# Kernel optimization log

Hardware: AMD Instinct MI355X
Metric: run time of the kernel (lower is better)

Reference implementation:

```python
import jax, jax.numpy as jnp
import numpy as np

B, T, IN, H, OUT = 128, 512, 64, 512, 1
H2 = H // 2


def setup_inputs() -> dict:
    key = jax.random.key(0)
    ks = jax.random.split(key, 16)
    s_in = 1.0 / np.sqrt(H)  # torch LSTM/Linear init scale ~ U(-1/sqrt(H), 1/sqrt(H))
    def u(k, shape, s):
        return jax.random.uniform(k, shape, jnp.float32, -s, s)
    return {
        "x": jax.random.normal(ks[0], (B, T, IN), jnp.float32),
        "W_ih0": u(ks[1], (4 * H, IN), s_in),
        "W_hh0": u(ks[2], (4 * H, H), s_in),
        "b_ih0": u(ks[3], (4 * H,), s_in),
        "b_hh0": u(ks[4], (4 * H,), s_in),
        "W_ih1": u(ks[5], (4 * H, H), s_in),
        "W_hh1": u(ks[6], (4 * H, H), s_in),
        "b_ih1": u(ks[7], (4 * H,), s_in),
        "b_hh1": u(ks[8], (4 * H,), s_in),
        "fc1_w": u(ks[9], (H2, H), s_in),
        "fc1_b": u(ks[10], (H2,), s_in),
        "fc2_w": u(ks[11], (OUT, H2), 1.0 / np.sqrt(H2)),
        "fc2_b": u(ks[12], (OUT,), 1.0 / np.sqrt(H2)),
    }


def _lstm_layer(x, W_ih, W_hh, b_ih, b_hh):
    # x: [B, T, D_in] -> outputs h for all timesteps [B, T, H]
    b, t, _ = x.shape
    h_dim = W_hh.shape[1]
    # precompute input contribution to gates for all timesteps: [T, B, 4H]
    xg = (jnp.einsum('btd,gd->btg', x, W_ih) + b_ih + b_hh).transpose(1, 0, 2)

    def step(carry, xt):
        h, c = carry
        gates = xt + h @ W_hh.T  # [B, 4H]
        i, f, g, o = jnp.split(gates, 4, axis=-1)  # torch gate order i,f,g,o
        i = jax.nn.sigmoid(i)
        f = jax.nn.sigmoid(f)
        g = jnp.tanh(g)
        o = jax.nn.sigmoid(o)
        c = f * c + i * g
        h = o * jnp.tanh(c)
        return (h, c), h

    h0 = jnp.zeros((b, h_dim), x.dtype)
    (_, _), hs = jax.lax.scan(step, (h0, h0), xg)
    return hs.transpose(1, 0, 2)  # [B, T, H]


def reference(x, W_ih0, W_hh0, b_ih0, b_hh0, W_ih1, W_hh1, b_ih1, b_hh1,
              fc1_w, fc1_b, fc2_w, fc2_b):
    h1 = _lstm_layer(x, W_ih0, W_hh0, b_ih0, b_hh0)
    h2 = _lstm_layer(h1, W_ih1, W_hh1, b_ih1, b_hh1)
    last = h2[:, -1, :]  # [B, H]
    z = jax.nn.relu(last @ fc1_w.T + fc1_b)
    return z @ fc2_w.T + fc2_b  # [B, OUT]
```

## Files before the change

kernel.cpp:

```cpp
#include <hip/hip_runtime.h>
#include <hip/hip_fp16.h>

#define BB   128
#define TT   512
#define INS  64
#define HH   512
#define K0   576
#define K1   1024
#define PAD0 584
#define PAD1 1032
#define NWG  128
#define NTHR 512
#define H2   256

typedef _Float16 f16;
typedef f16 f16x4 __attribute__((ext_vector_type(4)));
typedef f16 f16x8 __attribute__((ext_vector_type(8)));
typedef float f32x4 __attribute__((ext_vector_type(4)));

__device__ __forceinline__ float sigmoidf_(float x) {
  return 1.0f / (1.0f + __expf(-x));
}
__device__ __forceinline__ float tanhf_(float x) {
  return 1.0f - 2.0f / (__expf(2.0f * x) + 1.0f);
}

__device__ __forceinline__ f16x8 ldg_h(const f16* p) {
  union { unsigned long long q[2]; f16x8 v; } u;
  const unsigned long long* qp = (const unsigned long long*)p;
  u.q[0] = __hip_atomic_load(qp,     __ATOMIC_RELAXED, __HIP_MEMORY_SCOPE_AGENT);
  u.q[1] = __hip_atomic_load(qp + 1, __ATOMIC_RELAXED, __HIP_MEMORY_SCOPE_AGENT);
  return u.v;
}
__device__ __forceinline__ void stg_h(f16* p, unsigned int pk) {
  __hip_atomic_store((unsigned int*)p, pk, __ATOMIC_RELAXED, __HIP_MEMORY_SCOPE_AGENT);
}

__global__ __launch_bounds__(NTHR, 1) void lstm_fused(
    const float* __restrict__ x,
    const float* __restrict__ Wih0, const float* __restrict__ Whh0,
    const float* __restrict__ bih0, const float* __restrict__ bhh0,
    const float* __restrict__ Wih1, const float* __restrict__ Whh1,
    const float* __restrict__ bih1, const float* __restrict__ bhh1,
    int* __restrict__ bar, f16* __restrict__ h1buf, f16* __restrict__ h2buf)
{
  extern __shared__ f16 smem[];
  f16* W0s = smem;
  f16* W1s = smem + 32 * PAD0;

  const int tid  = threadIdx.x;
  const int wg   = blockIdx.x;
  const int mg   = wg >> 6;
  const int ng   = wg & 63;
  const int wid  = tid >> 6;
  const int lane = tid & 63;

  for (int e4 = tid; e4 < 32 * (K0 / 4); e4 += NTHR) {
    int r = e4 / (K0 / 4), k = (e4 - r * (K0 / 4)) * 4;
    int g = ((r >> 3) << 9) + (ng << 3) + (r & 7);
    float4 v = (k < INS)
        ? *reinterpret_cast<const float4*>(Wih0 + g * INS + k)
        : *reinterpret_cast<const float4*>(Whh0 + g * HH + (k - INS));
    f16x4 h; h[0]=(f16)v.x; h[1]=(f16)v.y; h[2]=(f16)v.z; h[3]=(f16)v.w;
    *reinterpret_cast<f16x4*>(&W0s[r * PAD0 + k]) = h;
  }
  for (int e4 = tid; e4 < 32 * (K1 / 4); e4 += NTHR) {
    int r = e4 >> 8, k = (e4 & 255) * 4;
    int g = ((r >> 3) << 9) + (ng << 3) + (r & 7);
    float4 v = (k < HH)
        ? *reinterpret_cast<const float4*>(Wih1 + g * HH + k)
        : *reinterpret_cast<const float4*>(Whh1 + g * HH + (k - HH));
    f16x4 h; h[0]=(f16)v.x; h[1]=(f16)v.y; h[2]=(f16)v.z; h[3]=(f16)v.w;
    *reinterpret_cast<f16x4*>(&W1s[r * PAD1 + k]) = h;
  }

  const bool isL1 = (wid >= 4);
  const int  wrow = mg * 64 + (wid & 3) * 16;
  const int  col0 = lane & 15;
  const int  rA   = lane & 15;
  const int  kq   = (lane >> 4) * 8;
  const int  hcol = (ng << 3) + (lane & 7);
  const bool low  = (lane & 8) == 0;
  const bool evn  = (lane & 1) == 0;

  float bias[2];
  #pragma unroll
  for (int n = 0; n < 2; n++) {
    int c = n * 16 + col0;
    int g = ((c >> 3) << 9) + (ng << 3) + (c & 7);
    bias[n] = isL1 ? (bih1[g] + bhh1[g]) : (bih0[g] + bhh0[g]);
  }
  __syncthreads();

  f32x4 cst = {};

  int* barh = bar + mg * 1024;
  int* grp  = barh + (ng & 7) * 64;
  int* glob = barh + 512;
  int* genp = barh + 576;

  for (int s = 0; s <= TT; ++s) {
    const f16* h1r = h1buf + ((s + 1) & 1) * (BB * HH);
    f16*       h1w = h1buf + ((s    ) & 1) * (BB * HH);
    const f16* h2r = h2buf + ((s    ) & 1) * (BB * HH);
    f16*       h2w = h2buf + ((s + 1) & 1) * (BB * HH);

    const bool active = isL1 ? (s >= 1) : (s < TT);
    if (active) {
      const int row = wrow + rA;
      f32x4 acc0 = {}, acc1 = {};

      if (!isL1) {
        const float* xb = x + ((size_t)row * TT + (size_t)s) * INS;
        #pragma unroll
        for (int ks = 0; ks < 2; ++ks) {
          const int kk = ks * 32 + kq;
          float4 q0 = *reinterpret_cast<const float4*>(xb + kk);
          float4 q1 = *reinterpret_cast<const float4*>(xb + kk + 4);
          f16x8 a;
          a[0]=(f16)q0.x; a[1]=(f16)q0.y; a[2]=(f16)q0.z; a[3]=(f16)q0.w;
          a[4]=(f16)q1.x; a[5]=(f16)q1.y; a[6]=(f16)q1.z; a[7]=(f16)q1.w;
          f16x8 b0 = *reinterpret_cast<const f16x8*>(&W0s[col0 * PAD0 + kk]);
          f16x8 b1 = *reinterpret_cast<const f16x8*>(&W0s[(16 + col0) * PAD0 + kk]);
          acc0 = __builtin_amdgcn_mfma_f32_16x16x32_f16(a, b0, acc0, 0, 0, 0);
          acc1 = __builtin_amdgcn_mfma_f32_16x16x32_f16(a, b1, acc1, 0, 0, 0);
        }
        #pragma unroll
        for (int c = 0; c < 2; ++c) {
          f16x8 a[8];
          #pragma unroll
          for (int u = 0; u < 8; ++u) {
            const int kh = (c * 8 + u) * 32 + kq;
            a[u] = ldg_h(h1r + row * HH + kh);
          }
          #pragma unroll
          for (int u = 0; u < 8; ++u) {
            const int kk = INS + (c * 8 + u) * 32 + kq;
            f16x8 b0 = *reinterpret_cast<const f16x8*>(&W0s[col0 * PAD0 + kk]);
            f16x8 b1 = *reinterpret_cast<const f16x8*>(&W0s[(16 + col0) * PAD0 + kk]);
            acc0 = __builtin_amdgcn_mfma_f32_16x16x32_f16(a[u], b0, acc0, 0, 0, 0);
            acc1 = __builtin_amdgcn_mfma_f32_16x16x32_f16(a[u], b1, acc1, 0, 0, 0);
          }
        }
      } else {
        #pragma unroll
        for (int c = 0; c < 4; ++c) {
          f16x8 a[8];
          #pragma unroll
          for (int u = 0; u < 8; ++u) {
            const int kk = (c * 8 + u) * 32 + kq;
            a[u] = (c < 2) ? ldg_h(h1r + row * HH + kk)
                           : ldg_h(h2r + row * HH + (kk - HH));
          }
          #pragma unroll
          for (int u = 0; u < 8; ++u) {
            const int kk = (c * 8 + u) * 32 + kq;
            f16x8 b0 = *reinterpret_cast<const f16x8*>(&W1s[col0 * PAD1 + kk]);
            f16x8 b1 = *reinterpret_cast<const f16x8*>(&W1s[(16 + col0) * PAD1 + kk]);
            acc0 = __builtin_amdgcn_mfma_f32_16x16x32_f16(a[u], b0, acc0, 0, 0, 0);
            acc1 = __builtin_amdgcn_mfma_f32_16x16x32_f16(a[u], b1, acc1, 0, 0, 0);
          }
        }
      }

      float res[4];
      #pragma unroll
      for (int j = 0; j < 4; j++) {
        float v0 = acc0[j] + bias[0];
        float v1 = acc1[j] + bias[1];
        float p0 = __shfl_xor(v0, 8, 64);
        float p1 = __shfl_xor(v1, 8, 64);
        float ip = low ? v0 : p0;
        float fp = low ? p0 : v0;
        float gp = low ? v1 : p1;
        float op = low ? p1 : v1;
        float cn = sigmoidf_(fp) * cst[j] + sigmoidf_(ip) * tanhf_(gp);
        cst[j] = cn;
        res[j] = sigmoidf_(op) * tanhf_(cn);
      }
      {
        f16* hw = isL1 ? h2w : h1w;
        const int rowb = wrow + ((lane >> 4) << 2);
        #pragma unroll
        for (int j = 0; j < 4; j++) {
          float other = __shfl_xor(res[j], 1, 64);
          if (low && evn) {
            f16 lo_ = (f16)res[j], hi_ = (f16)other;
            unsigned int pk =
                (unsigned int)__builtin_bit_cast(unsigned short, lo_) |
                ((unsigned int)__builtin_bit_cast(unsigned short, hi_) << 16);
            stg_h(hw + (rowb + j) * HH + hcol, pk);
          }
        }
      }
    }

    asm volatile("s_waitcnt vmcnt(0)" ::: "memory");
    __syncthreads();
    if (tid == 0) {
      int p = __hip_atomic_fetch_add(grp, 1, __ATOMIC_RELAXED, __HIP_MEMORY_SCOPE_AGENT);
      if ((p & 7) == 7) {
        int q = __hip_atomic_fetch_add(glob, 1, __ATOMIC_RELAXED, __HIP_MEMORY_SCOPE_AGENT);
        if ((q & 7) == 7)
          __hip_atomic_fetch_add(genp, 1, __ATOMIC_RELAXED, __HIP_MEMORY_SCOPE_AGENT);
      }
      while (__hip_atomic_load(genp, __ATOMIC_RELAXED, __HIP_MEMORY_SCOPE_AGENT) < s + 1)
        __builtin_amdgcn_s_sleep(1);
      asm volatile("" ::: "memory");
    }
    __syncthreads();
  }
}

__global__ void fc1_kernel(const f16* __restrict__ last, const float* __restrict__ w,
                           const float* __restrict__ b, float* __restrict__ z) {
  const int bb = blockIdx.x;
  const int j  = threadIdx.x;
  const f16*   lp = last + bb * HH;
  const float* wp = w + j * HH;
  float s = b[j];
  #pragma unroll 8
  for (int k = 0; k < HH; k++) s += (float)lp[k] * wp[k];
  z[bb * H2 + j] = fmaxf(s, 0.0f);
}

__global__ void fc2_kernel(const float* __restrict__ z, const float* __restrict__ w,
                           const float* __restrict__ b, float* __restrict__ out) {
  const int bb = threadIdx.x;
  float s = b[0];
  #pragma unroll 8
  for (int k = 0; k < H2; k++) s += z[bb * H2 + k] * w[k];
  out[bb] = s;
}

extern "C" void kernel_launch(void* const* d_in, const int* in_sizes, int n_in,
                              void* d_out, int out_size, void* d_ws, size_t ws_size,
                              hipStream_t stream) {
  const float* x     = (const float*)d_in[0];
  const float* Wih0  = (const float*)d_in[1];
  const float* Whh0  = (const float*)d_in[2];
  const float* bih0  = (const float*)d_in[3];
  const float* bhh0  = (const float*)d_in[4];
  const float* Wih1  = (const float*)d_in[5];
  const float* Whh1  = (const float*)d_in[6];
  const float* bih1  = (const float*)d_in[7];
  const float* bhh1  = (const float*)d_in[8];
  const float* fc1w  = (const float*)d_in[9];
  const float* fc1b  = (const float*)d_in[10];
  const float* fc2w  = (const float*)d_in[11];
  const float* fc2b  = (const float*)d_in[12];

  char* ws = (char*)d_ws;
  int*  bar = (int*)ws;
  f16*  h1  = (f16*)(ws + 8192);
  f16*  h2  = h1 + 2 * BB * HH;
  float* z  = (float*)(ws + 8192 + (size_t)4 * BB * HH * sizeof(f16));

  hipMemsetAsync(ws, 0, 8192 + (size_t)4 * BB * HH * sizeof(f16), stream);

  const size_t smem = (size_t)(32 * PAD0 + 32 * PAD1) * sizeof(f16);
  lstm_fused<<<NWG, NTHR, smem, stream>>>(x, Wih0, Whh0, bih0, bhh0,
                                          Wih1, Whh1, bih1, bhh1, bar, h1, h2);

  const f16* last = h2 + ((TT - 1) & 1) * (BB * HH);
  fc1_kernel<<<BB, 256, 0, stream>>>(last, fc1w, fc1b, z);
  fc2_kernel<<<1, BB, 0, stream>>>(z, fc2w, fc2b, (float*)d_out);
}
```

Baseline: 7.286 ms.

## Replace grid barrier with per-wave flag dataflow and split layers across workgroups

```diff
diff --git a/kernel.cpp b/kernel.cpp
--- a/kernel.cpp
+++ b/kernel.cpp
@@ -9,9 +9,9 @@
 #define K1   1024
 #define PAD0 584
 #define PAD1 1032
-#define NWG  128
-#define NTHR 512
 #define H2   256
+#define FS   16
+#define RING 4
 
 typedef _Float16 f16;
 typedef f16 f16x4 __attribute__((ext_vector_type(4)));
@@ -35,51 +35,57 @@
 __device__ __forceinline__ void stg_h(f16* p, unsigned int pk) {
   __hip_atomic_store((unsigned int*)p, pk, __ATOMIC_RELAXED, __HIP_MEMORY_SCOPE_AGENT);
 }
-
-__global__ __launch_bounds__(NTHR, 1) void lstm_fused(
+__device__ __forceinline__ int ldf(const int* p) {
+  return __hip_atomic_load(p, __ATOMIC_RELAXED, __HIP_MEMORY_SCOPE_AGENT);
+}
+
+__global__ __launch_bounds__(256, 1) void lstm_persist(
     const float* __restrict__ x,
     const float* __restrict__ Wih0, const float* __restrict__ Whh0,
     const float* __restrict__ bih0, const float* __restrict__ bhh0,
     const float* __restrict__ Wih1, const float* __restrict__ Whh1,
     const float* __restrict__ bih1, const float* __restrict__ bhh1,
-    int* __restrict__ bar, f16* __restrict__ h1buf, f16* __restrict__ h2buf)
+    int* __restrict__ flags, f16* __restrict__ h1ring, f16* __restrict__ h2ring)
 {
-  extern __shared__ f16 smem[];
-  f16* W0s = smem;
-  f16* W1s = smem + 32 * PAD0;
+  extern __shared__ f16 Ws[];
 
   const int tid  = threadIdx.x;
   const int wg   = blockIdx.x;
-  const int mg   = wg >> 6;
-  const int ng   = wg & 63;
+  const bool isL1 = (wg >= 128);
+  const int w2   = wg & 127;
+  const int mg   = w2 >> 6;
+  const int ng   = w2 & 63;
   const int wid  = tid >> 6;
   const int lane = tid & 63;
 
-  for (int e4 = tid; e4 < 32 * (K0 / 4); e4 += NTHR) {
-    int r = e4 / (K0 / 4), k = (e4 - r * (K0 / 4)) * 4;
-    int g = ((r >> 3) << 9) + (ng << 3) + (r & 7);
-    float4 v = (k < INS)
-        ? *reinterpret_cast<const float4*>(Wih0 + g * INS + k)
-        : *reinterpret_cast<const float4*>(Whh0 + g * HH + (k - INS));
-    f16x4 h; h[0]=(f16)v.x; h[1]=(f16)v.y; h[2]=(f16)v.z; h[3]=(f16)v.w;
-    *reinterpret_cast<f16x4*>(&W0s[r * PAD0 + k]) = h;
+  if (!isL1) {
+    for (int e4 = tid; e4 < 32 * (K0 / 4); e4 += 256) {
+      int r = e4 / (K0 / 4), k = (e4 - r * (K0 / 4)) * 4;
+      int g = ((r >> 3) << 9) + (ng << 3) + (r & 7);
+      float4 v = (k < INS)
+          ? *reinterpret_cast<const float4*>(Wih0 + g * INS + k)
+          : *reinterpret_cast<const float4*>(Whh0 + g * HH + (k - INS));
+      f16x4 h; h[0]=(f16)v.x; h[1]=(f16)v.y; h[2]=(f16)v.z; h[3]=(f16)v.w;
+      *reinterpret_cast<f16x4*>(&Ws[r * PAD0 + k]) = h;
+    }
+  } else {
+    for (int e4 = tid; e4 < 32 * (K1 / 4); e4 += 256) {
+      int r = e4 >> 8, k = (e4 & 255) * 4;
+      int g = ((r >> 3) << 9) + (ng << 3) + (r & 7);
+      float4 v = (k < HH)
+          ? *reinterpret_cast<const float4*>(Wih1 + g * HH + k)
+          : *reinterpret_cast<const float4*>(Whh1 + g * HH + (k - HH));
+      f16x4 h; h[0]=(f16)v.x; h[1]=(f16)v.y; h[2]=(f16)v.z; h[3]=(f16)v.w;
+      *reinterpret_cast<f16x4*>(&Ws[r * PAD1 + k]) = h;
+    }
   }
-  for (int e4 = tid; e4 < 32 * (K1 / 4); e4 += NTHR) {
-    int r = e4 >> 8, k = (e4 & 255) * 4;
-    int g = ((r >> 3) << 9) + (ng << 3) + (r & 7);
-    float4 v = (k < HH)
-        ? *reinterpret_cast<const float4*>(Wih1 + g * HH + k)
-        : *reinterpret_cast<const float4*>(Whh1 + g * HH + (k - HH));
-    f16x4 h; h[0]=(f16)v.x; h[1]=(f16)v.y; h[2]=(f16)v.z; h[3]=(f16)v.w;
-    *reinterpret_cast<f16x4*>(&W1s[r * PAD1 + k]) = h;
-  }
-
-  const bool isL1 = (wid >= 4);
-  const int  wrow = mg * 64 + (wid & 3) * 16;
+
+  const int  wrow = mg * 64 + wid * 16;
+  const int  row  = wrow + (lane & 15);
   const int  col0 = lane & 15;
-  const int  rA   = lane & 15;
   const int  kq   = (lane >> 4) * 8;
   const int  hcol = (ng << 3) + (lane & 7);
+  const int  rowb = wrow + ((lane >> 4) << 2);
   const bool low  = (lane & 8) == 0;
   const bool evn  = (lane & 1) == 0;
 
@@ -92,75 +98,68 @@
   }
   __syncthreads();
 
+  int* f1 = flags + (mg)     * 256 * FS;
+  int* f2 = flags + (2 + mg) * 256 * FS;
+  int* myflag = (isL1 ? f2 : f1) + (ng * 4 + wid) * FS;
+
   f32x4 cst = {};
 
-  int* barh = bar + mg * 1024;
-  int* grp  = barh + (ng & 7) * 64;
-  int* glob = barh + 512;
-  int* genp = barh + 576;
-
-  for (int s = 0; s <= TT; ++s) {
-    const f16* h1r = h1buf + ((s + 1) & 1) * (BB * HH);
-    f16*       h1w = h1buf + ((s    ) & 1) * (BB * HH);
-    const f16* h2r = h2buf + ((s    ) & 1) * (BB * HH);
-    f16*       h2w = h2buf + ((s + 1) & 1) * (BB * HH);
-
-    const bool active = isL1 ? (s >= 1) : (s < TT);
-    if (active) {
-      const int row = wrow + rA;
+  if (!isL1) {
+    for (int s = 0; s < TT; ++s) {
+      const f16* h1r = h1ring + ((s + RING - 1) & (RING - 1)) * (BB * HH);
+      f16*       h1w = h1ring + (s & (RING - 1)) * (BB * HH);
+
+      const float* xb = x + ((size_t)row * TT + (size_t)s) * INS;
+      float4 xq0 = *reinterpret_cast<const float4*>(xb + kq);
+      float4 xq1 = *reinterpret_cast<const float4*>(xb + kq + 4);
+      float4 xq2 = *reinterpret_cast<const float4*>(xb + 32 + kq);
+      float4 xq3 = *reinterpret_cast<const float4*>(xb + 32 + kq + 4);
+
+      int spin = 0;
+      for (;;) {
+        int m1 = ldf(f1 + (4 * lane + 0) * FS);
+        m1 = min(m1, ldf(f1 + (4 * lane + 1) * FS));
+        m1 = min(m1, ldf(f1 + (4 * lane + 2) * FS));
+        m1 = min(m1, ldf(f1 + (4 * lane + 3) * FS));
+        int m2 = ldf(f2 + (4 * lane + 0) * FS);
+        m2 = min(m2, ldf(f2 + (4 * lane + 1) * FS));
+        m2 = min(m2, ldf(f2 + (4 * lane + 2) * FS));
+        m2 = min(m2, ldf(f2 + (4 * lane + 3) * FS));
+        if (__all((m1 >= s) && (m2 >= s - 3))) break;
+        if (++spin > (1 << 16)) break;
+        __builtin_amdgcn_s_sleep(2);
+      }
+      asm volatile("" ::: "memory");
+
+      f16x8 a[16];
+      #pragma unroll
+      for (int u = 0; u < 16; ++u)
+        a[u] = ldg_h(h1r + row * HH + u * 32 + kq);
+
+      f16x8 ax0, ax1;
+      ax0[0]=(f16)xq0.x; ax0[1]=(f16)xq0.y; ax0[2]=(f16)xq0.z; ax0[3]=(f16)xq0.w;
+      ax0[4]=(f16)xq1.x; ax0[5]=(f16)xq1.y; ax0[6]=(f16)xq1.z; ax0[7]=(f16)xq1.w;
+      ax1[0]=(f16)xq2.x; ax1[1]=(f16)xq2.y; ax1[2]=(f16)xq2.z; ax1[3]=(f16)xq2.w;
+      ax1[4]=(f16)xq3.x; ax1[5]=(f16)xq3.y; ax1[6]=(f16)xq3.z; ax1[7]=(f16)xq3.w;
       f32x4 acc0 = {}, acc1 = {};
-
-      if (!isL1) {
-        const float* xb = x + ((size_t)row * TT + (size_t)s) * INS;
-        #pragma unroll
-        for (int ks = 0; ks < 2; ++ks) {
-          const int kk = ks * 32 + kq;
-          float4 q0 = *reinterpret_cast<const float4*>(xb + kk);
-          float4 q1 = *reinterpret_cast<const float4*>(xb + kk + 4);
-          f16x8 a;
-          a[0]=(f16)q0.x; a[1]=(f16)q0.y; a[2]=(f16)q0.z; a[3]=(f16)q0.w;
-          a[4]=(f16)q1.x; a[5]=(f16)q1.y; a[6]=(f16)q1.z; a[7]=(f16)q1.w;
-          f16x8 b0 = *reinterpret_cast<const f16x8*>(&W0s[col0 * PAD0 + kk]);
-          f16x8 b1 = *reinterpret_cast<const f16x8*>(&W0s[(16 + col0) * PAD0 + kk]);
-          acc0 = __builtin_amdgcn_mfma_f32_16x16x32_f16(a, b0, acc0, 0, 0, 0);
-          acc1 = __builtin_amdgcn_mfma_f32_16x16x32_f16(a, b1, acc1, 0, 0, 0);
-        }
-        #pragma unroll
-        for (int c = 0; c < 2; ++c) {
-          f16x8 a[8];
-          #pragma unroll
-          for (int u = 0; u < 8; ++u) {
-            const int kh = (c * 8 + u) * 32 + kq;
-            a[u] = ldg_h(h1r + row * HH + kh);
-          }
-          #pragma unroll
-          for (int u = 0; u < 8; ++u) {
-            const int kk = INS + (c * 8 + u) * 32 + kq;
-            f16x8 b0 = *reinterpret_cast<const f16x8*>(&W0s[col0 * PAD0 + kk]);
-            f16x8 b1 = *reinterpret_cast<const f16x8*>(&W0s[(16 + col0) * PAD0 + kk]);
-            acc0 = __builtin_amdgcn_mfma_f32_16x16x32_f16(a[u], b0, acc0, 0, 0, 0);
-            acc1 = __builtin_amdgcn_mfma_f32_16x16x32_f16(a[u], b1, acc1, 0, 0, 0);
-          }
-        }
-      } else {
-        #pragma unroll
-        for (int c = 0; c < 4; ++c) {
-          f16x8 a[8];
-          #pragma unroll
-          for (int u = 0; u < 8; ++u) {
-            const int kk = (c * 8 + u) * 32 + kq;
-            a[u] = (c < 2) ? ldg_h(h1r + row * HH + kk)
-                           : ldg_h(h2r + row * HH + (kk - HH));
-          }
-          #pragma unroll
-          for (int u = 0; u < 8; ++u) {
-            const int kk = (c * 8 + u) * 32 + kq;
-            f16x8 b0 = *reinterpret_cast<const f16x8*>(&W1s[col0 * PAD1 + kk]);
-            f16x8 b1 = *reinterpret_cast<const f16x8*>(&W1s[(16 + col0) * PAD1 + kk]);
-            acc0 = __builtin_amdgcn_mfma_f32_16x16x32_f16(a[u], b0, acc0, 0, 0, 0);
-            acc1 = __builtin_amdgcn_mfma_f32_16x16x32_f16(a[u], b1, acc1, 0, 0, 0);
-          }
-        }
+      {
+        f16x8 b;
+        b = *reinterpret_cast<const f16x8*>(&Ws[col0 * PAD0 + kq]);
+        acc0 = __builtin_amdgcn_mfma_f32_16x16x32_f16(ax0, b, acc0, 0, 0, 0);
+        b = *reinterpret_cast<const f16x8*>(&Ws[(16 + col0) * PAD0 + kq]);
+        acc1 = __builtin_amdgcn_mfma_f32_16x16x32_f16(ax0, b, acc1, 0, 0, 0);
+        b = *reinterpret_cast<const f16x8*>(&Ws[col0 * PAD0 + 32 + kq]);
+        acc0 = __builtin_amdgcn_mfma_f32_16x16x32_f16(ax1, b, acc0, 0, 0, 0);
+        b = *reinterpret_cast<const f16x8*>(&Ws[(16 + col0) * PAD0 + 32 + kq]);
+        acc1 = __builtin_amdgcn_mfma_f32_16x16x32_f16(ax1, b, acc1, 0, 0, 0);
+      }
+      #pragma unroll
+      for (int u = 0; u < 16; ++u) {
+        const int kk = INS + u * 32 + kq;
+        f16x8 b0 = *reinterpret_cast<const f16x8*>(&Ws[col0 * PAD0 + kk]);
+        f16x8 b1 = *reinterpret_cast<const f16x8*>(&Ws[(16 + col0) * PAD0 + kk]);
+        acc0 = __builtin_amdgcn_mfma_f32_16x16x32_f16(a[u], b0, acc0, 0, 0, 0);
+        acc1 = __builtin_amdgcn_mfma_f32_16x16x32_f16(a[u], b1, acc1, 0, 0, 0);
       }
 
       float res[4];
@@ -178,37 +177,91 @@
         cst[j] = cn;
         res[j] = sigmoidf_(op) * tanhf_(cn);
       }
-      {
-        f16* hw = isL1 ? h2w : h1w;
-        const int rowb = wrow + ((lane >> 4) << 2);
-        #pragma unroll
-        for (int j = 0; j < 4; j++) {
-          float other = __shfl_xor(res[j], 1, 64);
-          if (low && evn) {
-            f16 lo_ = (f16)res[j], hi_ = (f16)other;
-            unsigned int pk =
-                (unsigned int)__builtin_bit_cast(unsigned short, lo_) |
-                ((unsigned int)__builtin_bit_cast(unsigned short, hi_) << 16);
-            stg_h(hw + (rowb + j) * HH + hcol, pk);
-          }
+      #pragma unroll
+      for (int j = 0; j < 4; j++) {
+        float other = __shfl_xor(res[j], 1, 64);
+        if (low && evn) {
+          f16 lo_ = (f16)res[j], hi_ = (f16)other;
+          unsigned int pk =
+              (unsigned int)__builtin_bit_cast(unsigned short, lo_) |
+              ((unsigned int)__builtin_bit_cast(unsigned short, hi_) << 16);
+          stg_h(h1w + (rowb + j) * HH + hcol, pk);
         }
       }
+      asm volatile("s_waitcnt vmcnt(0)" ::: "memory");
+      if (lane == 0)
+        __hip_atomic_store(myflag, s + 1, __ATOMIC_RELAXED, __HIP_MEMORY_SCOPE_AGENT);
     }
-
-    asm volatile("s_waitcnt vmcnt(0)" ::: "memory");
-    __syncthreads();
-    if (tid == 0) {
-      int p = __hip_atomic_fetch_add(grp, 1, __ATOMIC_RELAXED, __HIP_MEMORY_SCOPE_AGENT);
-      if ((p & 7) == 7) {
-        int q = __hip_atomic_fetch_add(glob, 1, __ATOMIC_RELAXED, __HIP_MEMORY_SCOPE_AGENT);
-        if ((q & 7) == 7)
-          __hip_atomic_fetch_add(genp, 1, __ATOMIC_RELAXED, __HIP_MEMORY_SCOPE_AGENT);
-      }
-      while (__hip_atomic_load(genp, __ATOMIC_RELAXED, __HIP_MEMORY_SCOPE_AGENT) < s + 1)
-        __builtin_amdgcn_s_sleep(1);
+  } else {
+    for (int s = 1; s <= TT; ++s) {
+      const f16* h1r = h1ring + ((s + RING - 1) & (RING - 1)) * (BB * HH);
+      const f16* h2r = h2ring + ((s + RING - 2) & (RING - 1)) * (BB * HH);
+      f16*       h2w = h2ring + ((s + RING - 1) & (RING - 1)) * (BB * HH);
+
+      int spin = 0;
+      for (;;) {
+        int m1 = ldf(f1 + (4 * lane + 0) * FS);
+        m1 = min(m1, ldf(f1 + (4 * lane + 1) * FS));
+        m1 = min(m1, ldf(f1 + (4 * lane + 2) * FS));
+        m1 = min(m1, ldf(f1 + (4 * lane + 3) * FS));
+        int m2 = ldf(f2 + (4 * lane + 0) * FS);
+        m2 = min(m2, ldf(f2 + (4 * lane + 1) * FS));
+        m2 = min(m2, ldf(f2 + (4 * lane + 2) * FS));
+        m2 = min(m2, ldf(f2 + (4 * lane + 3) * FS));
+        if (__all((m1 >= s) && (m2 >= s - 1))) break;
+        if (++spin > (1 << 16)) break;
+        __builtin_amdgcn_s_sleep(2);
+      }
       asm volatile("" ::: "memory");
+
+      f16x8 a[32];
+      #pragma unroll
+      for (int u = 0; u < 16; ++u)
+        a[u] = ldg_h(h1r + row * HH + u * 32 + kq);
+      #pragma unroll
+      for (int u = 0; u < 16; ++u)
+        a[16 + u] = ldg_h(h2r + row * HH + u * 32 + kq);
+
+      f32x4 acc0 = {}, acc1 = {};
+      #pragma unroll
+      for (int u = 0; u < 32; ++u) {
+        const int kk = u * 32 + kq;
+        f16x8 b0 = *reinterpret_cast<const f16x8*>(&Ws[col0 * PAD1 + kk]);
+        f16x8 b1 = *reinterpret_cast<const f16x8*>(&Ws[(16 + col0) * PAD1 + kk]);
+        acc0 = __builtin_amdgcn_mfma_f32_16x16x32_f16(a[u], b0, acc0, 0, 0, 0);
+        acc1 = __builtin_amdgcn_mfma_f32_16x16x32_f16(a[u], b1, acc1, 0, 0, 0);
+      }
+
+      float res[4];
+      #pragma unroll
+      for (int j = 0; j < 4; j++) {
+        float v0 = acc0[j] + bias[0];
+        float v1 = acc1[j] + bias[1];
+        float p0 = __shfl_xor(v0, 8, 64);
+        float p1 = __shfl_xor(v1, 8, 64);
+        float ip = low ? v0 : p0;
+        float fp = low ? p0 : v0;
+        float gp = low ? v1 : p1;
+        float op = low ? p1 : v1;
+        float cn = sigmoidf_(fp) * cst[j] + sigmoidf_(ip) * tanhf_(gp);
+        cst[j] = cn;
+        res[j] = sigmoidf_(op) * tanhf_(cn);
+      }
+      #pragma unroll
+      for (int j = 0; j < 4; j++) {
+        float other = __shfl_xor(res[j], 1, 64);
+        if (low && evn) {
+          f16 lo_ = (f16)res[j], hi_ = (f16)other;
+          unsigned int pk =
+              (unsigned int)__builtin_bit_cast(unsigned short, lo_) |
+              ((unsigned int)__builtin_bit_cast(unsigned short, hi_) << 16);
+          stg_h(h2w + (rowb + j) * HH + hcol, pk);
+        }
+      }
+      asm volatile("s_waitcnt vmcnt(0)" ::: "memory");
+      if (lane == 0)
+        __hip_atomic_store(myflag, s, __ATOMIC_RELAXED, __HIP_MEMORY_SCOPE_AGENT);
     }
-    __syncthreads();
   }
 }
 
@@ -251,18 +304,19 @@
   const float* fc2b  = (const float*)d_in[12];
 
   char* ws = (char*)d_ws;
-  int*  bar = (int*)ws;
-  f16*  h1  = (f16*)(ws + 8192);
-  f16*  h2  = h1 + 2 * BB * HH;
-  float* z  = (float*)(ws + 8192 + (size_t)4 * BB * HH * sizeof(f16));
-
-  hipMemsetAsync(ws, 0, 8192 + (size_t)4 * BB * HH * sizeof(f16), stream);
-
-  const size_t smem = (size_t)(32 * PAD0 + 32 * PAD1) * sizeof(f16);
-  lstm_fused<<<NWG, NTHR, smem, stream>>>(x, Wih0, Whh0, bih0, bhh0,
-                                          Wih1, Whh1, bih1, bhh1, bar, h1, h2);
-
-  const f16* last = h2 + ((TT - 1) & 1) * (BB * HH);
+  int*  flags = (int*)ws;
+  const size_t FLAGS_B = (size_t)4 * 256 * FS * sizeof(int);
+  f16*  h1 = (f16*)(ws + FLAGS_B);
+  f16*  h2 = h1 + (size_t)RING * BB * HH;
+  float* z = (float*)(ws + FLAGS_B + (size_t)2 * RING * BB * HH * sizeof(f16));
+
+  hipMemsetAsync(ws, 0, FLAGS_B + (size_t)2 * RING * BB * HH * sizeof(f16), stream);
+
+  const size_t smem = (size_t)32 * PAD1 * sizeof(f16);
+  lstm_persist<<<256, 256, smem, stream>>>(x, Wih0, Whh0, bih0, bhh0,
+                                           Wih1, Whh1, bih1, bhh1, flags, h1, h2);
+
+  const f16* last = h2 + ((TT - 1) & (RING - 1)) * (BB * HH);
   fc1_kernel<<<BB, 256, 0, stream>>>(last, fc1w, fc1b, z);
   fc2_kernel<<<1, BB, 0, stream>>>(z, fc2w, fc2b, (float*)d_out);
 }
```

Result: slower. 8.392 ms (+15.2%).

## Restructure grid barrier into global tree with hierarchical wake and prefetched inputs

Applied to the files above, without the earlier changes.

```diff
diff --git a/kernel.cpp b/kernel.cpp
--- a/kernel.cpp
+++ b/kernel.cpp
@@ -12,6 +12,7 @@
 #define NWG  128
 #define NTHR 512
 #define H2   256
+#define FS   16
 
 typedef _Float16 f16;
 typedef f16 f16x4 __attribute__((ext_vector_type(4)));
@@ -35,6 +36,17 @@
 __device__ __forceinline__ void stg_h(f16* p, unsigned int pk) {
   __hip_atomic_store((unsigned int*)p, pk, __ATOMIC_RELAXED, __HIP_MEMORY_SCOPE_AGENT);
 }
+__device__ __forceinline__ int ldf(const int* p) {
+  return __hip_atomic_load(p, __ATOMIC_RELAXED, __HIP_MEMORY_SCOPE_AGENT);
+}
+
+#define FMA_BURST(bk)                                                     \
+  {                                                                       \
+    _Pragma("unroll")                                                     \
+    for (int i_ = 0; i_ < 64; i_++)                                       \
+      bk = __builtin_fmaf(bk, 1.0000001f, 1e-30f);                        \
+    asm volatile("" : "+v"(bk));                                          \
+  }
 
 __global__ __launch_bounds__(NTHR, 1) void lstm_fused(
     const float* __restrict__ x,
@@ -47,6 +59,7 @@
   extern __shared__ f16 smem[];
   f16* W0s = smem;
   f16* W1s = smem + 32 * PAD0;
+  __shared__ int smb;
 
   const int tid  = threadIdx.x;
   const int wg   = blockIdx.x;
@@ -54,6 +67,8 @@
   const int ng   = wg & 63;
   const int wid  = tid >> 6;
   const int lane = tid & 63;
+
+  if (tid == 0) smb = 0;
 
   for (int e4 = tid; e4 < 32 * (K0 / 4); e4 += NTHR) {
     int r = e4 / (K0 / 4), k = (e4 - r * (K0 / 4)) * 4;
@@ -92,12 +107,14 @@
   }
   __syncthreads();
 
+  int* grp   = bar + (wg & 15) * FS;
+  int* glob  = bar + 16 * FS;
+  int* genp  = bar + 17 * FS;
+  int* ggenp = bar + (18 + (wg >> 3)) * FS;
+  const bool head = ((wg & 7) == 0);
+
   f32x4 cst = {};
-
-  int* barh = bar + mg * 1024;
-  int* grp  = barh + (ng & 7) * 64;
-  int* glob = barh + 512;
-  int* genp = barh + 576;
+  float4 xpre0 = {}, xpre1 = {}, xpre2 = {}, xpre3 = {};
 
   for (int s = 0; s <= TT; ++s) {
     const f16* h1r = h1buf + ((s + 1) & 1) * (BB * HH);
@@ -105,25 +122,71 @@
     const f16* h2r = h2buf + ((s    ) & 1) * (BB * HH);
     f16*       h2w = h2buf + ((s + 1) & 1) * (BB * HH);
 
+    if (s > 0) {
+      if (!isL1 && s < TT) {
+        const float* xb = x + ((size_t)(wrow + rA) * TT + (size_t)s) * INS;
+        xpre0 = *reinterpret_cast<const float4*>(xb + kq);
+        xpre1 = *reinterpret_cast<const float4*>(xb + kq + 4);
+        xpre2 = *reinterpret_cast<const float4*>(xb + 32 + kq);
+        xpre3 = *reinterpret_cast<const float4*>(xb + 32 + kq + 4);
+      }
+      if (wid == 0) {
+        const int* pp = head ? genp : ggenp;
+        float bk = 1.0f;
+        int spin = 0;
+        for (;;) {
+          int v = (lane == 0) ? ldf(pp) : 0;
+          v = __shfl(v, 0, 64);
+          if (v >= s) break;
+          if (++spin > (1 << 17)) break;
+          FMA_BURST(bk);
+        }
+        if (head && lane == 0)
+          __hip_atomic_store(ggenp, s, __ATOMIC_RELAXED, __HIP_MEMORY_SCOPE_AGENT);
+        if (lane == 0)
+          __hip_atomic_store(&smb, s, __ATOMIC_RELAXED, __HIP_MEMORY_SCOPE_WORKGROUP);
+        asm volatile("" ::: "memory");
+      } else {
+        float bk = 1.0f;
+        int spin = 0;
+        while (__hip_atomic_load(&smb, __ATOMIC_RELAXED, __HIP_MEMORY_SCOPE_WORKGROUP) < s) {
+          if (++spin > (1 << 18)) break;
+          FMA_BURST(bk);
+        }
+        asm volatile("" ::: "memory");
+      }
+    }
+
     const bool active = isL1 ? (s >= 1) : (s < TT);
     if (active) {
       const int row = wrow + rA;
       f32x4 acc0 = {}, acc1 = {};
 
       if (!isL1) {
-        const float* xb = x + ((size_t)row * TT + (size_t)s) * INS;
-        #pragma unroll
-        for (int ks = 0; ks < 2; ++ks) {
-          const int kk = ks * 32 + kq;
-          float4 q0 = *reinterpret_cast<const float4*>(xb + kk);
-          float4 q1 = *reinterpret_cast<const float4*>(xb + kk + 4);
-          f16x8 a;
-          a[0]=(f16)q0.x; a[1]=(f16)q0.y; a[2]=(f16)q0.z; a[3]=(f16)q0.w;
-          a[4]=(f16)q1.x; a[5]=(f16)q1.y; a[6]=(f16)q1.z; a[7]=(f16)q1.w;
-          f16x8 b0 = *reinterpret_cast<const f16x8*>(&W0s[col0 * PAD0 + kk]);
-          f16x8 b1 = *reinterpret_cast<const f16x8*>(&W0s[(16 + col0) * PAD0 + kk]);
-          acc0 = __builtin_amdgcn_mfma_f32_16x16x32_f16(a, b0, acc0, 0, 0, 0);
-          acc1 = __builtin_amdgcn_mfma_f32_16x16x32_f16(a, b1, acc1, 0, 0, 0);
+        float4 q0, q1, q2, q3;
+        if (s > 0) { q0 = xpre0; q1 = xpre1; q2 = xpre2; q3 = xpre3; }
+        else {
+          const float* xb = x + ((size_t)row * TT + (size_t)s) * INS;
+          q0 = *reinterpret_cast<const float4*>(xb + kq);
+          q1 = *reinterpret_cast<const float4*>(xb + kq + 4);
+          q2 = *reinterpret_cast<const float4*>(xb + 32 + kq);
+          q3 = *reinterpret_cast<const float4*>(xb + 32 + kq + 4);
+        }
+        f16x8 ax0, ax1;
+        ax0[0]=(f16)q0.x; ax0[1]=(f16)q0.y; ax0[2]=(f16)q0.z; ax0[3]=(f16)q0.w;
+        ax0[4]=(f16)q1.x; ax0[5]=(f16)q1.y; ax0[6]=(f16)q1.z; ax0[7]=(f16)q1.w;
+        ax1[0]=(f16)q2.x; ax1[1]=(f16)q2.y; ax1[2]=(f16)q2.z; ax1[3]=(f16)q2.w;
+        ax1[4]=(f16)q3.x; ax1[5]=(f16)q3.y; ax1[6]=(f16)q3.z; ax1[7]=(f16)q3.w;
+        {
+          f16x8 b;
+          b = *reinterpret_cast<const f16x8*>(&W0s[col0 * PAD0 + kq]);
+          acc0 = __builtin_amdgcn_mfma_f32_16x16x32_f16(ax0, b, acc0, 0, 0, 0);
+          b = *reinterpret_cast<const f16x8*>(&W0s[(16 + col0) * PAD0 + kq]);
+          acc1 = __builtin_amdgcn_mfma_f32_16x16x32_f16(ax0, b, acc1, 0, 0, 0);
+          b = *reinterpret_cast<const f16x8*>(&W0s[col0 * PAD0 + 32 + kq]);
+          acc0 = __builtin_amdgcn_mfma_f32_16x16x32_f16(ax1, b, acc0, 0, 0, 0);
+          b = *reinterpret_cast<const f16x8*>(&W0s[(16 + col0) * PAD0 + 32 + kq]);
+          acc1 = __builtin_amdgcn_mfma_f32_16x16x32_f16(ax1, b, acc1, 0, 0, 0);
         }
         #pragma unroll
         for (int c = 0; c < 2; ++c) {
@@ -201,14 +264,10 @@
       int p = __hip_atomic_fetch_add(grp, 1, __ATOMIC_RELAXED, __HIP_MEMORY_SCOPE_AGENT);
       if ((p & 7) == 7) {
         int q = __hip_atomic_fetch_add(glob, 1, __ATOMIC_RELAXED, __HIP_MEMORY_SCOPE_AGENT);
-        if ((q & 7) == 7)
+        if ((q & 15) == 15)
           __hip_atomic_fetch_add(genp, 1, __ATOMIC_RELAXED, __HIP_MEMORY_SCOPE_AGENT);
       }
-      while (__hip_atomic_load(genp, __ATOMIC_RELAXED, __HIP_MEMORY_SCOPE_AGENT) < s + 1)
-        __builtin_amdgcn_s_sleep(1);
-      asm volatile("" ::: "memory");
     }
-    __syncthreads();
   }
 }
 
```

After: 8.004 ms. 9.9% more time.
